# Kernel tuning notes

Hardware: AMD Instinct MI355X
Metric: run time of the kernel (lower is better)

The kernel has to match this reference:

```python
import jax, jax.numpy as jnp
import numpy as np
from jax import lax

B_SZ, N_CH, N_T = 512, 129, 250
D_MODEL = 128
D_INNER = 256            # expand * d_model
D_STATE = 16
D_CONV = 4
HEADDIM = 64             # mamba_ssm default
NHEADS = D_INNER // HEADDIM  # 4
CONV_DIM = D_INNER + 2 * D_STATE        # 288 (ngroups=1)
D_IN_PROJ = 2 * D_INNER + 2 * D_STATE + NHEADS  # 548
EPS = 1e-5


def setup_inputs() -> dict:
    key = jax.random.key(0)
    ks = jax.random.split(key, 12)
    g = lambda k, shp, s: jax.random.normal(k, shp, jnp.float32) * s
    dt0 = jax.random.uniform(ks[4], (NHEADS,), minval=0.001, maxval=0.1)
    return {
        "x": jax.random.normal(ks[0], (B_SZ, N_CH, N_T), jnp.float32),
        "mixer_w": g(ks[1], (D_MODEL, N_CH), 0.05),
        "mixer_b": jnp.zeros((D_MODEL,), jnp.float32),
        "in_proj_w": g(ks[2], (D_IN_PROJ, D_MODEL), 0.05),
        "conv_w": g(ks[3], (CONV_DIM, D_CONV), 0.2),
        "conv_b": jnp.zeros((CONV_DIM,), jnp.float32),
        "dt_bias": jnp.log(jnp.expm1(dt0)),               # inverse-softplus init
        "A_log": jnp.log(jax.random.uniform(ks[5], (NHEADS,), minval=1.0, maxval=16.0)),
        "D": jnp.ones((NHEADS,), jnp.float32),
        "norm_w": jnp.ones((D_INNER,), jnp.float32),
        "out_proj_w": g(ks[6], (D_MODEL, D_INNER), 0.05),
        "head_w": g(ks[7], (1, D_MODEL), 0.05),
        "head_b": jnp.zeros((1,), jnp.float32),
    }


def reference(x, mixer_w, mixer_b, in_proj_w, conv_w, conv_b, dt_bias,
              A_log, D, norm_w, out_proj_w, head_w, head_b):
    bsz, _, T = x.shape
    # channel mixer: (B, C, T) -> (B, T, d_model)
    u = jnp.einsum('bct,dc->btd', x, mixer_w) + mixer_b
    # Mamba2 in_proj (no bias)
    zxbcdt = u @ in_proj_w.T                        # (B, T, 548)
    z = zxbcdt[..., :D_INNER]                       # gate
    xBC = zxbcdt[..., D_INNER:D_INNER + CONV_DIM]   # (B, T, 288)
    dt = jax.nn.softplus(zxbcdt[..., -NHEADS:] + dt_bias)  # (B, T, H)
    # causal depthwise conv1d (kernel 4) + SiLU
    pad = jnp.pad(xBC, ((0, 0), (D_CONV - 1, 0), (0, 0)))
    xBC = sum(conv_w[:, k] * pad[:, k:k + T, :] for k in range(D_CONV)) + conv_b
    xBC = jax.nn.silu(xBC)
    xh = xBC[..., :D_INNER].reshape(bsz, T, NHEADS, HEADDIM)
    Bm = xBC[..., D_INNER:D_INNER + D_STATE]        # (B, T, N)
    Cm = xBC[..., D_INNER + D_STATE:]               # (B, T, N)
    A = -jnp.exp(A_log)                             # (H,)
    dA = jnp.exp(dt * A)                            # (B, T, H)
    # selective state-space scan, time-major
    tm = lambda a: jnp.moveaxis(a, 1, 0)
    def step(h, inp):
        dA_t, dt_t, x_t, B_t, C_t = inp
        # h: (B, H, P, N)
        h = h * dA_t[:, :, None, None] + (dt_t[..., None] * x_t)[..., None] * B_t[:, None, None, :]
        y_t = jnp.einsum('bhpn,bn->bhp', h, C_t)
        return h, y_t
    h0 = jnp.zeros((bsz, NHEADS, HEADDIM, D_STATE), x.dtype)
    _, ys = lax.scan(step, h0, (tm(dA), tm(dt), tm(xh), tm(Bm), tm(Cm)))
    y = jnp.moveaxis(ys, 0, 1) + D[:, None] * xh    # skip connection, (B, T, H, P)
    y = y.reshape(bsz, T, D_INNER)
    # gated RMSNorm (norm_before_gate=False)
    y = y * jax.nn.silu(z)
    y = y * lax.rsqrt(jnp.mean(y * y, axis=-1, keepdims=True) + EPS) * norm_w
    y = y @ out_proj_w.T                            # (B, T, d_model)
    # head: AdaptiveAvgPool1d(1) over time -> Flatten -> Linear(d_model, 1)
    pooled = jnp.mean(y, axis=1)                    # (B, d_model)
    return pooled @ head_w.T + head_b               # (B, 1)
```

## Files before the change

### kernel.cpp

```cpp
#include <hip/hip_runtime.h>
#include <math.h>

#define NCH     129
#define NT      250
#define DINNER  256
#define DSTATE  16
#define NHEADS  4
#define DPROJ   548
#define TC      8
#define MT      35
#define KS4     4
#define ZR      17

typedef __attribute__((ext_vector_type(8))) short short8;
typedef __attribute__((ext_vector_type(4))) float f32x4;

template<int N> struct IC { static constexpr int value = N; };

__device__ __forceinline__ float silu_f(float x) { return x / (1.f + __expf(-x)); }

template<int CTRL>
__device__ __forceinline__ float dstep(float v) {
    int t = __builtin_amdgcn_update_dpp(0, __float_as_int(v), CTRL, 0xF, 0xF, true);
    return v + __int_as_float(t);
}
__device__ __forceinline__ float wave_sum63(float v) {
    v = dstep<0xB1>(v);  v = dstep<0x4E>(v);  v = dstep<0x141>(v);
    v = dstep<0x140>(v); v = dstep<0x142>(v); v = dstep<0x143>(v);
    return v;
}
__device__ __forceinline__ float rdlane(float v, int l) {
    return __uint_as_float(__builtin_amdgcn_readlane(__float_as_uint(v), l));
}
__device__ __forceinline__ unsigned short f2bf(float f) {
    unsigned u = __float_as_uint(f);
    u += 0x7FFF + ((u >> 16) & 1);
    return (unsigned short)(u >> 16);
}
__device__ __forceinline__ float bf2f(unsigned short h) {
    return __uint_as_float(((unsigned)h) << 16);
}

__global__ __launch_bounds__(256) void k_prep_w2(const float* __restrict__ in_proj_w,
                                                 const float* __restrict__ mixer_w,
                                                 const float* __restrict__ mixer_b,
                                                 float* __restrict__ w2t,
                                                 float* __restrict__ bias2) {
    int j = blockIdx.x;
    int c = threadIdx.x;
    if (c < NCH) {
        float acc = 0.f;
        for (int d = 0; d < 128; ++d)
            acc += in_proj_w[j * 128 + d] * mixer_w[d * NCH + c];
        w2t[(size_t)c * DPROJ + j] = acc;
    } else if (c == NCH) {
        float acc = 0.f;
        for (int d = 0; d < 128; ++d)
            acc += in_proj_w[j * 128 + d] * mixer_b[d];
        bias2[j] = acc;
    }
}

__global__ __launch_bounds__(256) void k_prep_v(const float* __restrict__ head_w,
                                                const float* __restrict__ out_proj_w,
                                                float* __restrict__ v) {
    int i = threadIdx.x;
    float acc = 0.f;
    for (int d = 0; d < 128; ++d)
        acc += head_w[d] * out_proj_w[(size_t)d * DINNER + i];
    v[i] = acc;
}

__global__ __launch_bounds__(64) void k_prep_frag(const float* __restrict__ w2t,
                                                  unsigned short* __restrict__ ahi,
                                                  unsigned short* __restrict__ alo) {
    int mt = blockIdx.x, ks = blockIdx.y;
    int lane = threadIdx.x;
    int m = mt * 16 + (lane & 15);
    size_t base = (((size_t)(mt * KS4 + ks)) * 64 + lane) * 8;
    for (int i = 0; i < 8; ++i) {
        int k = ks * 32 + (lane >> 4) * 8 + i;
        float v = (m < DPROJ) ? w2t[(size_t)k * DPROJ + m] : 0.f;
        unsigned short hb = f2bf(v);
        ahi[base + i] = hb;
        alo[base + i] = f2bf(v - bf2f(hb));
    }
}

__global__ __launch_bounds__(640, 1) void k_fused(
    const float* __restrict__ x,
    const unsigned short* __restrict__ ahi,
    const unsigned short* __restrict__ alo,
    const float* __restrict__ w2t,
    const float* __restrict__ bias2,
    const float* __restrict__ conv_w,
    const float* __restrict__ conv_b,
    const float* __restrict__ dt_bias,
    const float* __restrict__ A_log,
    const float* __restrict__ Dv,
    const float* __restrict__ norm_w,
    const float* __restrict__ vv,
    const float* __restrict__ head_b,
    float* __restrict__ out)
{
    __shared__ short xh[KS4 * 64 * 8];
    __shared__ short xl[KS4 * 64 * 8];
    __shared__ float x128buf[2][2][TC];
    __shared__ float zxbuf[DPROJ * ZR];
    __shared__ float bcbuf[2][TC][32];
    __shared__ float dtbuf[2][TC][NHEADS];
    __shared__ float dAbuf[2][TC][NHEADS];
    __shared__ float smp[2][2][TC][8];

    const int b2   = blockIdx.x;
    const int tid  = threadIdx.x;
    const int lane = tid & 63;
    const int wv   = tid >> 6;
    const bool isMain = (wv < 8);
    const int mb   = isMain ? (wv >> 2) : (wv - 8);
    const int p    = ((wv & 3) << 6) | lane;
    const int q    = lane;
    const int tcol = lane & 15;
    const int quad = lane >> 4;
    const bool isFold = isMain && ((wv & 3) == 0);

    const float* w128 = w2t + (size_t)128 * DPROJ;

    float bz = 0.f, bx = 0.f, w1z = 0.f, w1x = 0.f;
    float cw0 = 0.f, cw1 = 0.f, cw2 = 0.f, cw3 = 0.f, ccb = 0.f;
    float dtb = 0.f, Ah = 0.f, Dh = 0.f, nv = 0.f;
    if (isMain) {
        bz = bias2[p];          w1z = w128[p];
        bx = bias2[DINNER + p]; w1x = w128[DINNER + p];
        cw0 = conv_w[p * 4 + 0]; cw1 = conv_w[p * 4 + 1];
        cw2 = conv_w[p * 4 + 2]; cw3 = conv_w[p * 4 + 3];
        ccb = conv_b[p];
        Dh = Dv[p >> 6];
        nv = norm_w[p] * vv[p];
    } else if (q < 36) {
        bx  = bias2[2 * DINNER + q];
        w1x = w128[2 * DINNER + q];
        if (q < 32) {
            int ch = DINNER + q;
            cw0 = conv_w[ch * 4 + 0]; cw1 = conv_w[ch * 4 + 1];
            cw2 = conv_w[ch * 4 + 2]; cw3 = conv_w[ch * 4 + 3];
            ccb = conv_b[ch];
        } else {
            int h = q - 32;
            dtb = dt_bias[h];
            Ah  = -expf(A_log[h]);
        }
    }

    float za[TC], xa[TC], hs[DSTATE];
    float c1 = 0.f, c2 = 0.f, c3 = 0.f, outacc = 0.f;
#pragma unroll
    for (int n = 0; n < DSTATE; ++n) hs[n] = 0.f;

    const float* xb_aux = x + ((size_t)2 * b2 + mb) * NCH * NT;
    const int hh = wv & 3;
    float2 pr[9];

    auto load_chunk = [&](int t0, auto Lc) {
        constexpr int L  = decltype(Lc)::value;
        constexpr int HP = (L >= 2) ? L / 2 : 1;
        constexpr int PAIRS = NCH * HP;
#pragma unroll
        for (int k = 0; k * 64 < PAIRS; ++k) {
            int u = lane + 64 * k;
            if (u < PAIRS) {
                int c = u / HP, tp = u - c * HP;
                pr[k] = *(const float2*)(xb_aux + c * NT + t0 + 2 * tp);
            }
        }
    };
    auto store_chunk = [&](auto Lc, int nxtpar) {
        constexpr int L  = decltype(Lc)::value;
        constexpr int HP = (L >= 2) ? L / 2 : 1;
        constexpr int PAIRS = NCH * HP;
#pragma unroll
        for (int k = 0; k * 64 < PAIRS; ++k) {
            int u = lane + 64 * k;
            if (u < PAIRS) {
                int c = u / HP, tp = u - c * HP;
                float2 v = pr[k];
                if (c < 128) {
                    int base = ((c >> 5) * 64 + ((c >> 3) & 3) * 16) * 8 + (c & 7);
                    int col0 = mb * 8 + 2 * tp;
                    unsigned short h0 = f2bf(v.x), h1 = f2bf(v.y);
                    xh[base + col0 * 8]       = (short)h0;
                    xh[base + (col0 + 1) * 8] = (short)h1;
                    xl[base + col0 * 8]       = (short)f2bf(v.x - bf2f(h0));
                    xl[base + (col0 + 1) * 8] = (short)f2bf(v.y - bf2f(h1));
                } else {
                    x128buf[nxtpar][mb][2 * tp]     = v.x;
                    x128buf[nxtpar][mb][2 * tp + 1] = v.y;
                }
            }
        }
    };

    if (!isMain) { load_chunk(0, IC<TC>{}); store_chunk(IC<TC>{}, 0); }
    __syncthreads();

    auto stage = [&](auto CLc, auto NLc, int s) {
        constexpr int CL = decltype(CLc)::value;
        constexpr int NL = decltype(NLc)::value;
        const int cur = s & 1;

        if (isMain) {
            short8 bh[KS4], bl[KS4];
#pragma unroll
            for (int ks = 0; ks < KS4; ++ks) {
                bh[ks] = *(const short8*)&xh[(ks * 64 + lane) * 8];
                bl[ks] = *(const short8*)&xl[(ks * 64 + lane) * 8];
            }
            for (int mt = wv; mt < MT; mt += 8) {
                f32x4 a0 = {0.f, 0.f, 0.f, 0.f};
                f32x4 a1 = {0.f, 0.f, 0.f, 0.f};
#pragma unroll
                for (int ks = 0; ks < KS4; ++ks) {
                    size_t fo = (((size_t)(mt * KS4 + ks)) * 64 + lane) * 8;
                    short8 ah = *(const short8*)(ahi + fo);
                    short8 al = *(const short8*)(alo + fo);
                    a0 = __builtin_amdgcn_mfma_f32_16x16x32_bf16(ah, bh[ks], a0, 0, 0, 0);
                    a1 = __builtin_amdgcn_mfma_f32_16x16x32_bf16(ah, bl[ks], a1, 0, 0, 0);
                    a1 = __builtin_amdgcn_mfma_f32_16x16x32_bf16(al, bh[ks], a1, 0, 0, 0);
                }
#pragma unroll
                for (int r = 0; r < 4; ++r) {
                    int j = mt * 16 + quad * 4 + r;
                    if (j < DPROJ) zxbuf[j * ZR + tcol] = a0[r] + a1[r];
                }
            }
        } else {
            if constexpr (NL > 0) load_chunk((s + 1) * TC, IC<NL>{});
        }
        __syncthreads();

        if (isMain) {
            if (isFold && s > 0 && lane < TC) {
                const float* sp = smp[(s - 1) & 1][mb][lane];
                float s1 = sp[0] + sp[2] + sp[4] + sp[6];
                float s2 = sp[1] + sp[3] + sp[5] + sp[7];
                outacc = fmaf(s2, rsqrtf(fmaf(s1, 1.f / DINNER, 1e-5f)), outacc);
            }
#pragma unroll
            for (int tt = 0; tt < CL; ++tt) {
                float xm = x128buf[cur][mb][tt];
                int col = mb * 8 + tt;
                float zraw = zxbuf[p * ZR + col] + bz + w1z * xm;
                float xraw = zxbuf[(DINNER + p) * ZR + col] + bx + w1x * xm;
                float cv = fmaf(cw3, xraw, fmaf(cw2, c1, fmaf(cw1, c2, fmaf(cw0, c3, ccb))));
                c3 = c2; c2 = c1; c1 = xraw;
                xa[tt] = silu_f(cv);
                za[tt] = silu_f(zraw);
            }
        } else {
            if constexpr (NL > 0) store_chunk(IC<NL>{}, (s + 1) & 1);
            if (q < 32) {
#pragma unroll
                for (int tt = 0; tt < CL; ++tt) {
                    float xm = x128buf[cur][mb][tt];
                    float raw = zxbuf[(2 * DINNER + q) * ZR + mb * 8 + tt] + bx + w1x * xm;
                    float cv = fmaf(cw3, raw, fmaf(cw2, c1, fmaf(cw1, c2, fmaf(cw0, c3, ccb))));
                    c3 = c2; c2 = c1; c1 = raw;
                    bcbuf[mb][tt][q] = silu_f(cv);
                }
            } else if (q < 36) {
                int h = q - 32;
#pragma unroll
                for (int tt = 0; tt < CL; ++tt) {
                    float xm = x128buf[cur][mb][tt];
                    float val = zxbuf[(544 + h) * ZR + mb * 8 + tt] + bx + w1x * xm + dtb;
                    float dt = (val > 20.f) ? val : log1pf(expf(val));
                    dtbuf[mb][tt][h] = dt;
                    dAbuf[mb][tt][h] = __expf(dt * Ah);
                }
            }
        }
        __syncthreads();

        if (isMain) {
#pragma unroll
            for (int tt = 0; tt < CL; ++tt) {
                float xv  = xa[tt];
                float g   = za[tt];
                float dtv = dtbuf[mb][tt][hh];
                float dAv = dAbuf[mb][tt][hh];
                float bcv = bcbuf[mb][tt][lane & 31];
                float dx = dtv * xv;
                float y0 = 0.f, y1 = 0.f, y2 = 0.f, y3 = 0.f;
#pragma unroll
                for (int n = 0; n < 4; ++n) {
                    float b0 = rdlane(bcv, n),      cc0 = rdlane(bcv, DSTATE + n);
                    float b1 = rdlane(bcv, 4 + n),  cc1 = rdlane(bcv, DSTATE + 4 + n);
                    float b2v = rdlane(bcv, 8 + n), cc2 = rdlane(bcv, DSTATE + 8 + n);
                    float b3 = rdlane(bcv, 12 + n), cc3 = rdlane(bcv, DSTATE + 12 + n);
                    hs[n]      = fmaf(hs[n],      dAv, dx * b0);  y0 = fmaf(hs[n],      cc0, y0);
                    hs[4 + n]  = fmaf(hs[4 + n],  dAv, dx * b1);  y1 = fmaf(hs[4 + n],  cc1, y1);
                    hs[8 + n]  = fmaf(hs[8 + n],  dAv, dx * b2v); y2 = fmaf(hs[8 + n],  cc2, y2);
                    hs[12 + n] = fmaf(hs[12 + n], dAv, dx * b3);  y3 = fmaf(hs[12 + n], cc3, y3);
                }
                float val = fmaf(Dh, xv, (y0 + y1) + (y2 + y3)) * g;
                float s1 = wave_sum63(val * val);
                float s2 = wave_sum63(val * nv);
                if (lane == 63) {
                    smp[cur][mb][tt][2 * (wv & 3)]     = s1;
                    smp[cur][mb][tt][2 * (wv & 3) + 1] = s2;
                }
            }
        }
    };

    stage(IC<8>{}, IC<8>{}, 0);
    for (int s = 1; s <= 29; ++s) stage(IC<8>{}, IC<8>{}, s);
    stage(IC<8>{}, IC<2>{}, 30);
    stage(IC<2>{}, IC<0>{}, 31);
    __syncthreads();

    if (isFold) {
        if (lane < 2) {
            const float* sp = smp[1][mb][lane];
            float s1 = sp[0] + sp[2] + sp[4] + sp[6];
            float s2 = sp[1] + sp[3] + sp[5] + sp[7];
            outacc = fmaf(s2, rsqrtf(fmaf(s1, 1.f / DINNER, 1e-5f)), outacc);
        }
        float tot = wave_sum63(outacc);
        if (lane == 63) out[2 * b2 + mb] = head_b[0] + tot * (1.f / NT);
    }
}

extern "C" void kernel_launch(void* const* d_in, const int* in_sizes, int n_in,
                              void* d_out, int out_size, void* d_ws, size_t ws_size,
                              hipStream_t stream) {
    const float* x         = (const float*)d_in[0];
    const float* mixer_w   = (const float*)d_in[1];
    const float* mixer_b   = (const float*)d_in[2];
    const float* in_proj_w = (const float*)d_in[3];
    const float* conv_w    = (const float*)d_in[4];
    const float* conv_b    = (const float*)d_in[5];
    const float* dt_bias   = (const float*)d_in[6];
    const float* A_log     = (const float*)d_in[7];
    const float* Dp        = (const float*)d_in[8];
    const float* norm_w    = (const float*)d_in[9];
    const float* out_proj_w= (const float*)d_in[10];
    const float* head_w    = (const float*)d_in[11];
    const float* head_b    = (const float*)d_in[12];
    float* out = (float*)d_out;

    int B = in_sizes[0] / (NCH * NT);

    float* ws    = (float*)d_ws;
    float* w2t   = ws;
    float* bias2 = w2t + (size_t)NCH * DPROJ;
    float* vvp   = bias2 + DPROJ;
    unsigned short* ahi = (unsigned short*)(vvp + DINNER);
    unsigned short* alo = ahi + (size_t)MT * KS4 * 64 * 8;

    k_prep_w2<<<DPROJ, 256, 0, stream>>>(in_proj_w, mixer_w, mixer_b, w2t, bias2);
    k_prep_v<<<1, 256, 0, stream>>>(head_w, out_proj_w, vvp);
    k_prep_frag<<<dim3(MT, KS4), 64, 0, stream>>>(w2t, ahi, alo);
    k_fused<<<B / 2, 640, 0, stream>>>(x, ahi, alo, w2t, bias2, conv_w, conv_b,
                                       dt_bias, A_log, Dp, norm_w, vvp, head_b, out);
}
```

Baseline: 442.8 us.

## Switch to 32x32 MFMA with 16-step time chunks and merge prep kernels

Time-chunk size doubles from 8 to 16, so the per-block projection GEMM now uses 32x32x16 bf16 MFMA tiles covering 32 columns (16 steps for each of the two batch elements). That halves the number of stages and barriers. The dedicated loader waves are removed: all 8 waves share the x loading and scattering, and B/C/dt computation moves into one wave per batch element. The three prep kernels are merged into one that writes MFMA fragments directly, cutting launches. In exchange each thread holds more registers per chunk (za/xa of 16), and the scan waves now also carry load and scatter work.

```diff
diff --git a/kernel.cpp b/kernel.cpp
--- a/kernel.cpp
+++ b/kernel.cpp
@@ -7,13 +7,13 @@
 #define DSTATE  16
 #define NHEADS  4
 #define DPROJ   548
-#define TC      8
-#define MT      35
-#define KS4     4
-#define ZR      17
-
-typedef __attribute__((ext_vector_type(8))) short short8;
-typedef __attribute__((ext_vector_type(4))) float f32x4;
+#define TC      16
+#define NMT     18
+#define NKS     8
+#define ZR      33
+
+typedef __attribute__((ext_vector_type(8)))  short short8;
+typedef __attribute__((ext_vector_type(16))) float f32x16;
 
 template<int N> struct IC { static constexpr int value = N; };
 
@@ -41,58 +41,65 @@
     return __uint_as_float(((unsigned)h) << 16);
 }
 
-__global__ __launch_bounds__(256) void k_prep_w2(const float* __restrict__ in_proj_w,
-                                                 const float* __restrict__ mixer_w,
-                                                 const float* __restrict__ mixer_b,
-                                                 float* __restrict__ w2t,
-                                                 float* __restrict__ bias2) {
-    int j = blockIdx.x;
-    int c = threadIdx.x;
-    if (c < NCH) {
+__global__ __launch_bounds__(256) void k_prep(
+    const float* __restrict__ in_proj_w,
+    const float* __restrict__ mixer_w,
+    const float* __restrict__ mixer_b,
+    const float* __restrict__ head_w,
+    const float* __restrict__ out_proj_w,
+    unsigned short* __restrict__ ahi,
+    unsigned short* __restrict__ alo,
+    float* __restrict__ bias2,
+    float* __restrict__ w128,
+    float* __restrict__ vvp)
+{
+    int blk = blockIdx.x;
+    int t = threadIdx.x;
+    if (blk < NMT * NKS) {
+        int mt = blk >> 3, ks = blk & 7;
+        int lane = t & 63, sub = t >> 6;
+        int m = mt * 32 + (lane & 31);
+#pragma unroll
+        for (int ii = 0; ii < 2; ++ii) {
+            int i = sub * 2 + ii;
+            int k = ks * 16 + (lane >> 5) * 8 + i;
+            float acc = 0.f;
+            if (m < DPROJ)
+                for (int d = 0; d < 128; ++d)
+                    acc += in_proj_w[m * 128 + d] * mixer_w[d * NCH + k];
+            unsigned short hb = f2bf(acc);
+            size_t o = (((size_t)(mt * NKS + ks)) * 64 + lane) * 8 + i;
+            ahi[o] = hb;
+            alo[o] = f2bf(acc - bf2f(hb));
+        }
+    } else if (blk == NMT * NKS) {
+#pragma unroll
+        for (int r = 0; r < 3; ++r) {
+            int j = (r == 0) ? t : (r == 1) ? t + 256 : 512 + t;
+            if (r == 2 && t >= 36) break;
+            float ab = 0.f, aw = 0.f;
+            for (int d = 0; d < 128; ++d) {
+                float w = in_proj_w[j * 128 + d];
+                ab += w * mixer_b[d];
+                aw += w * mixer_w[d * NCH + 128];
+            }
+            bias2[j] = ab;
+            w128[j]  = aw;
+        }
+    } else {
         float acc = 0.f;
         for (int d = 0; d < 128; ++d)
-            acc += in_proj_w[j * 128 + d] * mixer_w[d * NCH + c];
-        w2t[(size_t)c * DPROJ + j] = acc;
-    } else if (c == NCH) {
-        float acc = 0.f;
-        for (int d = 0; d < 128; ++d)
-            acc += in_proj_w[j * 128 + d] * mixer_b[d];
-        bias2[j] = acc;
+            acc += head_w[d] * out_proj_w[d * DINNER + t];
+        vvp[t] = acc;
     }
 }
 
-__global__ __launch_bounds__(256) void k_prep_v(const float* __restrict__ head_w,
-                                                const float* __restrict__ out_proj_w,
-                                                float* __restrict__ v) {
-    int i = threadIdx.x;
-    float acc = 0.f;
-    for (int d = 0; d < 128; ++d)
-        acc += head_w[d] * out_proj_w[(size_t)d * DINNER + i];
-    v[i] = acc;
-}
-
-__global__ __launch_bounds__(64) void k_prep_frag(const float* __restrict__ w2t,
-                                                  unsigned short* __restrict__ ahi,
-                                                  unsigned short* __restrict__ alo) {
-    int mt = blockIdx.x, ks = blockIdx.y;
-    int lane = threadIdx.x;
-    int m = mt * 16 + (lane & 15);
-    size_t base = (((size_t)(mt * KS4 + ks)) * 64 + lane) * 8;
-    for (int i = 0; i < 8; ++i) {
-        int k = ks * 32 + (lane >> 4) * 8 + i;
-        float v = (m < DPROJ) ? w2t[(size_t)k * DPROJ + m] : 0.f;
-        unsigned short hb = f2bf(v);
-        ahi[base + i] = hb;
-        alo[base + i] = f2bf(v - bf2f(hb));
-    }
-}
-
-__global__ __launch_bounds__(640, 1) void k_fused(
+__global__ __launch_bounds__(512, 1) void k_fused(
     const float* __restrict__ x,
     const unsigned short* __restrict__ ahi,
     const unsigned short* __restrict__ alo,
-    const float* __restrict__ w2t,
     const float* __restrict__ bias2,
+    const float* __restrict__ w128,
     const float* __restrict__ conv_w,
     const float* __restrict__ conv_b,
     const float* __restrict__ dt_bias,
@@ -103,104 +110,103 @@
     const float* __restrict__ head_b,
     float* __restrict__ out)
 {
-    __shared__ short xh[KS4 * 64 * 8];
-    __shared__ short xl[KS4 * 64 * 8];
-    __shared__ float x128buf[2][2][TC];
+    __shared__ short xh[NKS * 64 * 8];
+    __shared__ short xl[NKS * 64 * 8];
     __shared__ float zxbuf[DPROJ * ZR];
     __shared__ float bcbuf[2][TC][32];
     __shared__ float dtbuf[2][TC][NHEADS];
     __shared__ float dAbuf[2][TC][NHEADS];
+    __shared__ float x128buf[2][2][TC];
     __shared__ float smp[2][2][TC][8];
 
     const int b2   = blockIdx.x;
     const int tid  = threadIdx.x;
     const int lane = tid & 63;
     const int wv   = tid >> 6;
-    const bool isMain = (wv < 8);
-    const int mb   = isMain ? (wv >> 2) : (wv - 8);
-    const int p    = ((wv & 3) << 6) | lane;
-    const int q    = lane;
-    const int tcol = lane & 15;
-    const int quad = lane >> 4;
-    const bool isFold = isMain && ((wv & 3) == 0);
-
-    const float* w128 = w2t + (size_t)128 * DPROJ;
-
-    float bz = 0.f, bx = 0.f, w1z = 0.f, w1x = 0.f;
-    float cw0 = 0.f, cw1 = 0.f, cw2 = 0.f, cw3 = 0.f, ccb = 0.f;
-    float dtb = 0.f, Ah = 0.f, Dh = 0.f, nv = 0.f;
-    if (isMain) {
-        bz = bias2[p];          w1z = w128[p];
-        bx = bias2[DINNER + p]; w1x = w128[DINNER + p];
-        cw0 = conv_w[p * 4 + 0]; cw1 = conv_w[p * 4 + 1];
-        cw2 = conv_w[p * 4 + 2]; cw3 = conv_w[p * 4 + 3];
-        ccb = conv_b[p];
-        Dh = Dv[p >> 6];
-        nv = norm_w[p] * vv[p];
-    } else if (q < 36) {
-        bx  = bias2[2 * DINNER + q];
-        w1x = w128[2 * DINNER + q];
-        if (q < 32) {
-            int ch = DINNER + q;
-            cw0 = conv_w[ch * 4 + 0]; cw1 = conv_w[ch * 4 + 1];
-            cw2 = conv_w[ch * 4 + 2]; cw3 = conv_w[ch * 4 + 3];
-            ccb = conv_b[ch];
+    const int mb   = wv >> 2;
+    const int wq   = wv & 3;
+    const int p    = (wq << 6) | lane;
+    const bool isBC   = (wq == 1) && (lane < 36);
+    const bool isFold = (wq == 0);
+
+    float bz = bias2[p], bx = bias2[DINNER + p];
+    float w1z = w128[p], w1x = w128[DINNER + p];
+    float cw0 = conv_w[p * 4 + 0], cw1 = conv_w[p * 4 + 1];
+    float cw2 = conv_w[p * 4 + 2], cw3 = conv_w[p * 4 + 3];
+    float ccb = conv_b[p];
+    float Dh  = Dv[wq];
+    float nv  = norm_w[p] * vv[p];
+    float bxb = 0.f, w1b = 0.f, e0 = 0.f, e1 = 0.f, e2 = 0.f, e3 = 0.f, eb = 0.f;
+    float dtb = 0.f, Ah = 0.f;
+    if (isBC) {
+        bxb = bias2[512 + lane]; w1b = w128[512 + lane];
+        if (lane < 32) {
+            int ch = DINNER + lane;
+            e0 = conv_w[ch * 4 + 0]; e1 = conv_w[ch * 4 + 1];
+            e2 = conv_w[ch * 4 + 2]; e3 = conv_w[ch * 4 + 3];
+            eb = conv_b[ch];
         } else {
-            int h = q - 32;
-            dtb = dt_bias[h];
-            Ah  = -expf(A_log[h]);
+            dtb = dt_bias[lane - 32];
+            Ah  = -expf(A_log[lane - 32]);
         }
     }
 
     float za[TC], xa[TC], hs[DSTATE];
-    float c1 = 0.f, c2 = 0.f, c3 = 0.f, outacc = 0.f;
+    float c1 = 0.f, c2 = 0.f, c3 = 0.f;
+    float g1 = 0.f, g2 = 0.f, g3 = 0.f;
+    float outacc = 0.f;
 #pragma unroll
     for (int n = 0; n < DSTATE; ++n) hs[n] = 0.f;
 
-    const float* xb_aux = x + ((size_t)2 * b2 + mb) * NCH * NT;
-    const int hh = wv & 3;
-    float2 pr[9];
+    const float* xbase = x + (size_t)2 * b2 * NCH * NT;
+    float2 pr[5];
 
     auto load_chunk = [&](int t0, auto Lc) {
         constexpr int L  = decltype(Lc)::value;
-        constexpr int HP = (L >= 2) ? L / 2 : 1;
-        constexpr int PAIRS = NCH * HP;
-#pragma unroll
-        for (int k = 0; k * 64 < PAIRS; ++k) {
-            int u = lane + 64 * k;
-            if (u < PAIRS) {
-                int c = u / HP, tp = u - c * HP;
-                pr[k] = *(const float2*)(xb_aux + c * NT + t0 + 2 * tp);
+        constexpr int HP = L / 2;
+        constexpr int NP = NCH * HP;
+#pragma unroll
+        for (int k = 0; k * 512 < 2 * NP; ++k) {
+            int g = tid + 512 * k;
+            if (g < 2 * NP) {
+                int mbx = (g >= NP) ? 1 : 0;
+                int rem = g - mbx * NP;
+                int c = rem / HP, tp = rem - c * HP;
+                pr[k] = *(const float2*)(xbase + (size_t)mbx * NCH * NT + c * NT + t0 + 2 * tp);
             }
         }
     };
-    auto store_chunk = [&](auto Lc, int nxtpar) {
+    auto scatter_chunk = [&](auto Lc, int par) {
         constexpr int L  = decltype(Lc)::value;
-        constexpr int HP = (L >= 2) ? L / 2 : 1;
-        constexpr int PAIRS = NCH * HP;
-#pragma unroll
-        for (int k = 0; k * 64 < PAIRS; ++k) {
-            int u = lane + 64 * k;
-            if (u < PAIRS) {
-                int c = u / HP, tp = u - c * HP;
+        constexpr int HP = L / 2;
+        constexpr int NP = NCH * HP;
+#pragma unroll
+        for (int k = 0; k * 512 < 2 * NP; ++k) {
+            int g = tid + 512 * k;
+            if (g < 2 * NP) {
+                int mbx = (g >= NP) ? 1 : 0;
+                int rem = g - mbx * NP;
+                int c = rem / HP, tp = rem - c * HP;
                 float2 v = pr[k];
                 if (c < 128) {
-                    int base = ((c >> 5) * 64 + ((c >> 3) & 3) * 16) * 8 + (c & 7);
-                    int col0 = mb * 8 + 2 * tp;
+                    int ks = c >> 4, half = (c >> 3) & 1, i = c & 7;
+                    int col = mbx * 16 + 2 * tp;
+                    int pos = (ks * 64 + half * 32 + col) * 8 + i;
                     unsigned short h0 = f2bf(v.x), h1 = f2bf(v.y);
-                    xh[base + col0 * 8]       = (short)h0;
-                    xh[base + (col0 + 1) * 8] = (short)h1;
-                    xl[base + col0 * 8]       = (short)f2bf(v.x - bf2f(h0));
-                    xl[base + (col0 + 1) * 8] = (short)f2bf(v.y - bf2f(h1));
+                    xh[pos]     = (short)h0;
+                    xh[pos + 8] = (short)h1;
+                    xl[pos]     = (short)f2bf(v.x - bf2f(h0));
+                    xl[pos + 8] = (short)f2bf(v.y - bf2f(h1));
                 } else {
-                    x128buf[nxtpar][mb][2 * tp]     = v.x;
-                    x128buf[nxtpar][mb][2 * tp + 1] = v.y;
+                    x128buf[par][mbx][2 * tp]     = v.x;
+                    x128buf[par][mbx][2 * tp + 1] = v.y;
                 }
             }
         }
     };
 
-    if (!isMain) { load_chunk(0, IC<TC>{}); store_chunk(IC<TC>{}, 0); }
+    load_chunk(0, IC<TC>{});
+    scatter_chunk(IC<TC>{}, 0);
     __syncthreads();
 
     auto stage = [&](auto CLc, auto NLc, int s) {
@@ -208,71 +214,63 @@
         constexpr int NL = decltype(NLc)::value;
         const int cur = s & 1;
 
-        if (isMain) {
-            short8 bh[KS4], bl[KS4];
-#pragma unroll
-            for (int ks = 0; ks < KS4; ++ks) {
-                bh[ks] = *(const short8*)&xh[(ks * 64 + lane) * 8];
-                bl[ks] = *(const short8*)&xl[(ks * 64 + lane) * 8];
-            }
-            for (int mt = wv; mt < MT; mt += 8) {
-                f32x4 a0 = {0.f, 0.f, 0.f, 0.f};
-                f32x4 a1 = {0.f, 0.f, 0.f, 0.f};
-#pragma unroll
-                for (int ks = 0; ks < KS4; ++ks) {
-                    size_t fo = (((size_t)(mt * KS4 + ks)) * 64 + lane) * 8;
-                    short8 ah = *(const short8*)(ahi + fo);
-                    short8 al = *(const short8*)(alo + fo);
-                    a0 = __builtin_amdgcn_mfma_f32_16x16x32_bf16(ah, bh[ks], a0, 0, 0, 0);
-                    a1 = __builtin_amdgcn_mfma_f32_16x16x32_bf16(ah, bl[ks], a1, 0, 0, 0);
-                    a1 = __builtin_amdgcn_mfma_f32_16x16x32_bf16(al, bh[ks], a1, 0, 0, 0);
-                }
-#pragma unroll
-                for (int r = 0; r < 4; ++r) {
-                    int j = mt * 16 + quad * 4 + r;
-                    if (j < DPROJ) zxbuf[j * ZR + tcol] = a0[r] + a1[r];
-                }
-            }
-        } else {
-            if constexpr (NL > 0) load_chunk((s + 1) * TC, IC<NL>{});
+        if constexpr (NL > 0) load_chunk((s + 1) * TC, IC<NL>{});
+        for (int mt = wv; mt < NMT; mt += 8) {
+            f32x16 a0 = {0.f,0.f,0.f,0.f,0.f,0.f,0.f,0.f,0.f,0.f,0.f,0.f,0.f,0.f,0.f,0.f};
+            f32x16 a1 = {0.f,0.f,0.f,0.f,0.f,0.f,0.f,0.f,0.f,0.f,0.f,0.f,0.f,0.f,0.f,0.f};
+#pragma unroll
+            for (int ks = 0; ks < NKS; ++ks) {
+                size_t fo = (((size_t)(mt * NKS + ks)) * 64 + lane) * 8;
+                short8 ah  = *(const short8*)(ahi + fo);
+                short8 al  = *(const short8*)(alo + fo);
+                short8 bhv = *(const short8*)&xh[(ks * 64 + lane) * 8];
+                short8 blv = *(const short8*)&xl[(ks * 64 + lane) * 8];
+                a0 = __builtin_amdgcn_mfma_f32_32x32x16_bf16(ah, bhv, a0, 0, 0, 0);
+                a1 = __builtin_amdgcn_mfma_f32_32x32x16_bf16(ah, blv, a1, 0, 0, 0);
+                a1 = __builtin_amdgcn_mfma_f32_32x32x16_bf16(al, bhv, a1, 0, 0, 0);
+            }
+#pragma unroll
+            for (int r = 0; r < 16; ++r) {
+                int j = mt * 32 + (r & 3) + 8 * (r >> 2) + 4 * (lane >> 5);
+                if (j < DPROJ) zxbuf[j * ZR + (lane & 31)] = a0[r] + a1[r];
+            }
         }
         __syncthreads();
 
-        if (isMain) {
-            if (isFold && s > 0 && lane < TC) {
-                const float* sp = smp[(s - 1) & 1][mb][lane];
-                float s1 = sp[0] + sp[2] + sp[4] + sp[6];
-                float s2 = sp[1] + sp[3] + sp[5] + sp[7];
-                outacc = fmaf(s2, rsqrtf(fmaf(s1, 1.f / DINNER, 1e-5f)), outacc);
-            }
-#pragma unroll
-            for (int tt = 0; tt < CL; ++tt) {
-                float xm = x128buf[cur][mb][tt];
-                int col = mb * 8 + tt;
-                float zraw = zxbuf[p * ZR + col] + bz + w1z * xm;
-                float xraw = zxbuf[(DINNER + p) * ZR + col] + bx + w1x * xm;
-                float cv = fmaf(cw3, xraw, fmaf(cw2, c1, fmaf(cw1, c2, fmaf(cw0, c3, ccb))));
-                c3 = c2; c2 = c1; c1 = xraw;
-                xa[tt] = silu_f(cv);
-                za[tt] = silu_f(zraw);
-            }
-        } else {
-            if constexpr (NL > 0) store_chunk(IC<NL>{}, (s + 1) & 1);
-            if (q < 32) {
+        if constexpr (NL > 0) scatter_chunk(IC<NL>{}, (s + 1) & 1);
+        if (isFold && s > 0 && lane < TC) {
+            const float* sp = smp[(s - 1) & 1][mb][lane];
+            float s1 = sp[0] + sp[2] + sp[4] + sp[6];
+            float s2 = sp[1] + sp[3] + sp[5] + sp[7];
+            outacc = fmaf(s2, rsqrtf(fmaf(s1, 1.f / DINNER, 1e-5f)), outacc);
+        }
+#pragma unroll
+        for (int tt = 0; tt < CL; ++tt) {
+            float xm = x128buf[cur][mb][tt];
+            int col = mb * 16 + tt;
+            float zraw = zxbuf[p * ZR + col] + bz + w1z * xm;
+            float xraw = zxbuf[(DINNER + p) * ZR + col] + bx + w1x * xm;
+            float cv = fmaf(cw3, xraw, fmaf(cw2, c1, fmaf(cw1, c2, fmaf(cw0, c3, ccb))));
+            c3 = c2; c2 = c1; c1 = xraw;
+            xa[tt] = silu_f(cv);
+            za[tt] = silu_f(zraw);
+        }
+        if (isBC) {
+            if (lane < 32) {
 #pragma unroll
                 for (int tt = 0; tt < CL; ++tt) {
                     float xm = x128buf[cur][mb][tt];
-                    float raw = zxbuf[(2 * DINNER + q) * ZR + mb * 8 + tt] + bx + w1x * xm;
-                    float cv = fmaf(cw3, raw, fmaf(cw2, c1, fmaf(cw1, c2, fmaf(cw0, c3, ccb))));
-                    c3 = c2; c2 = c1; c1 = raw;
-                    bcbuf[mb][tt][q] = silu_f(cv);
+                    float raw = zxbuf[(512 + lane) * ZR + mb * 16 + tt] + bxb + w1b * xm;
+                    float cv = fmaf(e3, raw, fmaf(e2, g1, fmaf(e1, g2, fmaf(e0, g3, eb))));
+                    g3 = g2; g2 = g1; g1 = raw;
+                    bcbuf[mb][tt][lane] = silu_f(cv);
                 }
-            } else if (q < 36) {
-                int h = q - 32;
+            } else {
+                int h = lane - 32;
 #pragma unroll
                 for (int tt = 0; tt < CL; ++tt) {
                     float xm = x128buf[cur][mb][tt];
-                    float val = zxbuf[(544 + h) * ZR + mb * 8 + tt] + bx + w1x * xm + dtb;
+                    float val = zxbuf[(544 + h) * ZR + mb * 16 + tt] + bxb + w1b * xm + dtb;
                     float dt = (val > 20.f) ? val : log1pf(expf(val));
                     dtbuf[mb][tt][h] = dt;
                     dAbuf[mb][tt][h] = __expf(dt * Ah);
@@ -281,46 +279,43 @@
         }
         __syncthreads();
 
-        if (isMain) {
-#pragma unroll
-            for (int tt = 0; tt < CL; ++tt) {
-                float xv  = xa[tt];
-                float g   = za[tt];
-                float dtv = dtbuf[mb][tt][hh];
-                float dAv = dAbuf[mb][tt][hh];
-                float bcv = bcbuf[mb][tt][lane & 31];
-                float dx = dtv * xv;
-                float y0 = 0.f, y1 = 0.f, y2 = 0.f, y3 = 0.f;
-#pragma unroll
-                for (int n = 0; n < 4; ++n) {
-                    float b0 = rdlane(bcv, n),      cc0 = rdlane(bcv, DSTATE + n);
-                    float b1 = rdlane(bcv, 4 + n),  cc1 = rdlane(bcv, DSTATE + 4 + n);
-                    float b2v = rdlane(bcv, 8 + n), cc2 = rdlane(bcv, DSTATE + 8 + n);
-                    float b3 = rdlane(bcv, 12 + n), cc3 = rdlane(bcv, DSTATE + 12 + n);
-                    hs[n]      = fmaf(hs[n],      dAv, dx * b0);  y0 = fmaf(hs[n],      cc0, y0);
-                    hs[4 + n]  = fmaf(hs[4 + n],  dAv, dx * b1);  y1 = fmaf(hs[4 + n],  cc1, y1);
-                    hs[8 + n]  = fmaf(hs[8 + n],  dAv, dx * b2v); y2 = fmaf(hs[8 + n],  cc2, y2);
-                    hs[12 + n] = fmaf(hs[12 + n], dAv, dx * b3);  y3 = fmaf(hs[12 + n], cc3, y3);
-                }
-                float val = fmaf(Dh, xv, (y0 + y1) + (y2 + y3)) * g;
-                float s1 = wave_sum63(val * val);
-                float s2 = wave_sum63(val * nv);
-                if (lane == 63) {
-                    smp[cur][mb][tt][2 * (wv & 3)]     = s1;
-                    smp[cur][mb][tt][2 * (wv & 3) + 1] = s2;
-                }
+#pragma unroll
+        for (int tt = 0; tt < CL; ++tt) {
+            float xv  = xa[tt];
+            float g   = za[tt];
+            float dtv = dtbuf[mb][tt][wq];
+            float dAv = dAbuf[mb][tt][wq];
+            float bcv = bcbuf[mb][tt][lane & 31];
+            float dx = dtv * xv;
+            float y0 = 0.f, y1 = 0.f, y2 = 0.f, y3 = 0.f;
+#pragma unroll
+            for (int n = 0; n < 4; ++n) {
+                float b0 = rdlane(bcv, n),      cc0 = rdlane(bcv, DSTATE + n);
+                float b1 = rdlane(bcv, 4 + n),  cc1 = rdlane(bcv, DSTATE + 4 + n);
+                float b2v = rdlane(bcv, 8 + n), cc2 = rdlane(bcv, DSTATE + 8 + n);
+                float b3 = rdlane(bcv, 12 + n), cc3 = rdlane(bcv, DSTATE + 12 + n);
+                hs[n]      = fmaf(hs[n],      dAv, dx * b0);  y0 = fmaf(hs[n],      cc0, y0);
+                hs[4 + n]  = fmaf(hs[4 + n],  dAv, dx * b1);  y1 = fmaf(hs[4 + n],  cc1, y1);
+                hs[8 + n]  = fmaf(hs[8 + n],  dAv, dx * b2v); y2 = fmaf(hs[8 + n],  cc2, y2);
+                hs[12 + n] = fmaf(hs[12 + n], dAv, dx * b3);  y3 = fmaf(hs[12 + n], cc3, y3);
+            }
+            float val = fmaf(Dh, xv, (y0 + y1) + (y2 + y3)) * g;
+            float s1 = wave_sum63(val * val);
+            float s2 = wave_sum63(val * nv);
+            if (lane == 63) {
+                smp[cur][mb][tt][2 * wq]     = s1;
+                smp[cur][mb][tt][2 * wq + 1] = s2;
             }
         }
     };
 
-    stage(IC<8>{}, IC<8>{}, 0);
-    for (int s = 1; s <= 29; ++s) stage(IC<8>{}, IC<8>{}, s);
-    stage(IC<8>{}, IC<2>{}, 30);
-    stage(IC<2>{}, IC<0>{}, 31);
+    for (int s = 0; s <= 13; ++s) stage(IC<16>{}, IC<16>{}, s);
+    stage(IC<16>{}, IC<10>{}, 14);
+    stage(IC<10>{}, IC<0>{},  15);
     __syncthreads();
 
     if (isFold) {
-        if (lane < 2) {
+        if (lane < 10) {
             const float* sp = smp[1][mb][lane];
             float s1 = sp[0] + sp[2] + sp[4] + sp[6];
             float s2 = sp[1] + sp[3] + sp[5] + sp[7];
@@ -351,16 +346,16 @@
 
     int B = in_sizes[0] / (NCH * NT);
 
-    float* ws    = (float*)d_ws;
-    float* w2t   = ws;
-    float* bias2 = w2t + (size_t)NCH * DPROJ;
-    float* vvp   = bias2 + DPROJ;
-    unsigned short* ahi = (unsigned short*)(vvp + DINNER);
-    unsigned short* alo = ahi + (size_t)MT * KS4 * 64 * 8;
-
-    k_prep_w2<<<DPROJ, 256, 0, stream>>>(in_proj_w, mixer_w, mixer_b, w2t, bias2);
-    k_prep_v<<<1, 256, 0, stream>>>(head_w, out_proj_w, vvp);
-    k_prep_frag<<<dim3(MT, KS4), 64, 0, stream>>>(w2t, ahi, alo);
-    k_fused<<<B / 2, 640, 0, stream>>>(x, ahi, alo, w2t, bias2, conv_w, conv_b,
+    const size_t FRAG = (size_t)NMT * NKS * 64 * 8;
+    unsigned short* ahi = (unsigned short*)d_ws;
+    unsigned short* alo = ahi + FRAG;
+    float* bias2 = (float*)(alo + FRAG);
+    float* w128  = bias2 + DPROJ;
+    float* vvp   = w128 + DPROJ;
+
+    k_prep<<<NMT * NKS + 2, 256, 0, stream>>>(in_proj_w, mixer_w, mixer_b,
+                                              head_w, out_proj_w,
+                                              ahi, alo, bias2, w128, vvp);
+    k_fused<<<B / 2, 512, 0, stream>>>(x, ahi, alo, bias2, w128, conv_w, conv_b,
                                        dt_bias, A_log, Dp, norm_w, vvp, head_b, out);
 }
```

After: 433.3 us. 2.1% less time.
